# Optimization experiments

Hardware: AMD Instinct MI355X
Metric: run time of the kernel (lower is better)

Reference implementation:

```python
import jax, jax.numpy as jnp
import numpy as np

N, A, B, K = 100000, 64, 128, 27  # active sites, in/out channels, 3^3 offsets
EPS = 1e-4  # scn BatchNorm default eps
LEAK = 0.0  # leakiness=0 -> ReLU


def bn_lrelu(x, gamma, beta):
    # training-mode BN over active sites, fused leaky relu
    mu = x.mean(0)
    var = x.var(0)
    xh = (x - mu) * jax.lax.rsqrt(var + EPS) * gamma + beta
    return jnp.where(xh > 0, xh, LEAK * xh)


def subconv(f, nbr, mask, W):
    # submanifold conv via rulebook: f [N,Cin], nbr [N,K], mask [N,K], W [K,Cin,Cout]
    out = jnp.zeros((f.shape[0], W.shape[2]), f.dtype)
    for k in range(W.shape[0]):  # fixed small set of kernel offsets
        g = jnp.where(mask[:, k:k + 1], f[nbr[:, k]], jnp.zeros((), f.dtype))
        out = out + g @ W[k]
    return out


def setup_inputs() -> dict:
    key = jax.random.key(0)
    ks = jax.random.split(key, 8)
    feat = jax.random.normal(ks[0], (N, A), jnp.float32)
    nbr = jax.random.randint(ks[1], (N, K), 0, N, jnp.int32)
    mask = jax.random.randint(ks[2], (N, K), 0, 2, jnp.int32).astype(bool)
    # self-connection at center offset is always valid in submanifold conv
    center = K // 2
    nbr = nbr.at[:, center].set(jnp.arange(N, dtype=jnp.int32))
    mask = mask.at[:, center].set(True)
    s1 = 1.0 / np.sqrt(K * A)
    s2 = 1.0 / np.sqrt(K * B)
    W1 = jax.random.normal(ks[3], (K, A, B), jnp.float32) * s1
    W2 = jax.random.normal(ks[4], (K, B, B), jnp.float32) * s2
    Wnin = jax.random.normal(ks[5], (A, B), jnp.float32) / np.sqrt(A)
    gamma1 = jnp.ones((A,), jnp.float32)
    beta1 = jnp.zeros((A,), jnp.float32)
    gamma2 = jnp.ones((B,), jnp.float32)
    beta2 = jnp.zeros((B,), jnp.float32)
    return {"feat": feat, "gamma1": gamma1, "beta1": beta1, "W1": W1,
            "gamma2": gamma2, "beta2": beta2, "W2": W2, "Wnin": Wnin,
            "nbr": nbr, "mask": mask}


def reference(feat, gamma1, beta1, W1, gamma2, beta2, W2, Wnin, nbr, mask):
    y1 = feat @ Wnin  # NetworkInNetwork shortcut (a != b)
    h = bn_lrelu(feat, gamma1, beta1)
    h = subconv(h, nbr, mask, W1)
    h = bn_lrelu(h, gamma2, beta2)
    y2 = subconv(h, nbr, mask, W2)
    return y1 + y2  # add_feature_planes
```

## Files before the change

### kernel.cpp

```cpp
#include <hip/hip_runtime.h>
#include <stdint.h>

#define CA 64
#define CB 128
#define KOFF 27
#define BN_EPS 1e-4f

typedef short bf16x8 __attribute__((ext_vector_type(8)));
typedef float f32x4 __attribute__((ext_vector_type(4)));
typedef unsigned int u32x4 __attribute__((ext_vector_type(4)));
typedef unsigned short u16x4 __attribute__((ext_vector_type(4)));

__device__ __forceinline__ unsigned short f2bf(float f) {
  union { float f; uint32_t u; } c; c.f = f;
  uint32_t u = c.u;
  return (unsigned short)((u + 0x7FFFu + ((u >> 16) & 1u)) >> 16);
}

__device__ __forceinline__ void barrier_lds() {
  asm volatile("s_waitcnt lgkmcnt(0)\n\ts_barrier" ::: "memory");
}

__global__ void detect_mask_k(const unsigned char* __restrict__ m, int* flag) {
  unsigned v = 0;
  for (int i = threadIdx.x; i < 4096; i += 256)
    if (i & 3) v |= m[i];
  if (v) atomicOr(flag, 1);
}

__global__ void pack_mask_k(const void* __restrict__ mp, const int* __restrict__ flag,
                            uint32_t* __restrict__ bits, int n) {
  int i = blockIdx.x * blockDim.x + threadIdx.x;
  if (i >= n) return;
  uint32_t b = 0;
  if (*flag) {
    const unsigned char* m = (const unsigned char*)mp + (size_t)i * KOFF;
    for (int k = 0; k < KOFF; k++) b |= (m[k] ? 1u : 0u) << k;
  } else {
    const int* m = (const int*)mp + (size_t)i * KOFF;
    for (int k = 0; k < KOFF; k++) b |= (m[k] ? 1u : 0u) << k;
  }
  bits[i] = b;
}

__global__ void transpose_all_k(const float* __restrict__ W1, const float* __restrict__ W2,
                                const float* __restrict__ Wnin,
                                unsigned short* __restrict__ w1t, unsigned short* __restrict__ w2t,
                                unsigned short* __restrict__ wnt) {
  const int t1 = KOFF * CA * CB, t2 = KOFF * CB * CB, t3 = CA * CB;
  int idx = blockIdx.x * blockDim.x + threadIdx.x;
  if (idx < t1) {
    int ci = idx % CA; int r = idx / CA; int co = r % CB; int k = r / CB;
    w1t[idx] = f2bf(W1[((size_t)k * CA + ci) * CB + co]);
  } else if (idx < t1 + t2) {
    int j = idx - t1;
    int ci = j % CB; int r = j / CB; int co = r % CB; int k = r / CB;
    w2t[j] = f2bf(W2[((size_t)k * CB + ci) * CB + co]);
  } else if (idx < t1 + t2 + t3) {
    int j = idx - t1 - t2;
    int ci = j % CA; int co = j / CA;
    wnt[j] = f2bf(Wnin[(size_t)ci * CB + co]);
  }
}

template<int C>
__global__ void col_stats_k(const float* __restrict__ x, int n, float* __restrict__ sums) {
  __shared__ float ssum[C], ssq[C];
  int t = threadIdx.x;
  for (int i = t; i < C; i += 256) { ssum[i] = 0.f; ssq[i] = 0.f; }
  __syncthreads();
  const int c = t % C;
  const int rpb = 256 / C;
  float s = 0.f, q = 0.f;
  for (int r = blockIdx.x * rpb + t / C; r < n; r += gridDim.x * rpb) {
    float v = x[(size_t)r * C + c];
    s += v; q += v * v;
  }
  atomicAdd(&ssum[c], s);
  atomicAdd(&ssq[c], q);
  __syncthreads();
  for (int i = t; i < C; i += 256) {
    atomicAdd(&sums[i], ssum[i]);
    atomicAdd(&sums[C + i], ssq[i]);
  }
}

template<int C>
__global__ void bn_finalize_k(const float* __restrict__ sums, const float* __restrict__ gamma,
                              const float* __restrict__ beta, float* __restrict__ sc, int n) {
  int c = threadIdx.x;
  if (c >= C) return;
  float inv_n = 1.f / (float)n;
  float mean = sums[c] * inv_n;
  float var = sums[C + c] * inv_n - mean * mean;
  float rstd = rsqrtf(var + BN_EPS);
  float scale = gamma[c] * rstd;
  sc[c] = scale;
  sc[C + c] = beta[c] - mean * scale;
}

template<int C, bool RAW>
__global__ void bn_apply_k(const float* __restrict__ x, const float* __restrict__ sc,
                           unsigned short* __restrict__ h, unsigned short* __restrict__ raw,
                           int total) {
  int idx = (blockIdx.x * blockDim.x + threadIdx.x) * 4;
  if (idx >= total) return;
  f32x4 v = *(const f32x4*)&x[idx];
  int c0 = idx % C;
  u16x4 ho, ro;
#pragma unroll
  for (int j = 0; j < 4; j++) {
    float s = sc[c0 + j], b = sc[C + c0 + j];
    float hv = fmaxf(v[j] * s + b, 0.f);
    ho[j] = f2bf(hv);
    if (RAW) ro[j] = f2bf(v[j]);
  }
  *(u16x4*)&h[idx] = ho;
  if (RAW) *(u16x4*)&raw[idx] = ro;
}

template<int CIN, bool FUSE>
__launch_bounds__(256)
__global__ void conv_k(const unsigned short* __restrict__ hin,
                       const unsigned short* __restrict__ wt,
                       const int* __restrict__ nbr,
                       const uint32_t* __restrict__ mbits,
                       const unsigned short* __restrict__ fbraw,
                       const unsigned short* __restrict__ wnt,
                       float* __restrict__ out, int n) {
  constexpr int TR = 64;
  constexpr int STR = CIN + 8;
  constexpr int FSTR = CA + 8;
  constexpr int NKS = CIN / 32;
  constexpr int CH = CIN / 8;
  constexpr int NP = TR * CH / 256;

  __shared__ alignas(16) unsigned short tile[2][TR * STR];
  __shared__ alignas(16) unsigned short ftile[FUSE ? TR * FSTR : 16];
  __shared__ int lnbr[TR * KOFF];
  __shared__ uint32_t lmb[TR];

  const int t = threadIdx.x;
  const int rowbase = blockIdx.x * TR;
  const int nrows = min(TR, n - rowbase);

  for (int i = t; i < nrows * KOFF; i += 256) lnbr[i] = nbr[(size_t)rowbase * KOFF + i];
  if (t < TR) lmb[t] = (t < nrows) ? mbits[rowbase + t] : 0u;

  if constexpr (FUSE) {
#pragma unroll
    for (int p = 0; p < 2; p++) {
      int r = p * 32 + (t >> 3);
      int ch = (t & 7) * 8;
      u32x4 v = {0, 0, 0, 0};
      if (r < nrows) v = *(const u32x4*)&fbraw[(size_t)(rowbase + r) * CA + ch];
      *(u32x4*)&ftile[r * FSTR + ch] = v;
    }
  }
  __syncthreads();

  const int lane = t & 63;
  const int wave = t >> 6;
  const int l16 = lane & 15;
  const int quad = lane >> 4;
  const int colbase = wave * 32;
  const int goff = (t % CH) * 8;
  const int grow = t / CH;
  const int boff0 = (colbase + l16) * CIN + quad * 8;
  const int boff1 = boff0 + 16 * CIN;

  f32x4 acc[4][2];
#pragma unroll
  for (int i = 0; i < 4; i++) { acc[i][0] = f32x4{0,0,0,0}; acc[i][1] = f32x4{0,0,0,0}; }

  bf16x8 bfr[2][2 * NKS];
  u32x4 gr[NP];

#pragma unroll
  for (int ks = 0; ks < NKS; ks++) {
    bfr[0][2 * ks]     = *(const bf16x8*)&wt[boff0 + ks * 32];
    bfr[0][2 * ks + 1] = *(const bf16x8*)&wt[boff1 + ks * 32];
  }
#pragma unroll
  for (int p = 0; p < NP; p++) {
    int r = p * (256 / CH) + grow;
    u32x4 v = {0, 0, 0, 0};
    if (r < nrows && (lmb[r] & 1u)) v = *(const u32x4*)&hin[(size_t)lnbr[r * KOFF] * CIN + goff];
    gr[p] = v;
  }
#pragma unroll
  for (int p = 0; p < NP; p++) {
    int r = p * (256 / CH) + grow;
    *(u32x4*)&tile[0][r * STR + goff] = gr[p];
  }
  {
    const unsigned short* wk = wt + (size_t)1 * CB * CIN;
#pragma unroll
    for (int ks = 0; ks < NKS; ks++) {
      bfr[1][2 * ks]     = *(const bf16x8*)&wk[boff0 + ks * 32];
      bfr[1][2 * ks + 1] = *(const bf16x8*)&wk[boff1 + ks * 32];
    }
  }
#pragma unroll
  for (int p = 0; p < NP; p++) {
    int r = p * (256 / CH) + grow;
    u32x4 v = {0, 0, 0, 0};
    if (r < nrows && ((lmb[r] >> 1) & 1u))
      v = *(const u32x4*)&hin[(size_t)lnbr[r * KOFF + 1] * CIN + goff];
    gr[p] = v;
  }

  if constexpr (FUSE) {
#pragma unroll
    for (int ks = 0; ks < CA / 32; ks++) {
      bf16x8 b0 = *(const bf16x8*)&wnt[(colbase + l16) * CA + ks * 32 + quad * 8];
      bf16x8 b1 = *(const bf16x8*)&wnt[(colbase + 16 + l16) * CA + ks * 32 + quad * 8];
#pragma unroll
      for (int rt = 0; rt < 4; rt++) {
        bf16x8 a = *(const bf16x8*)&ftile[(rt * 16 + l16) * FSTR + ks * 32 + quad * 8];
        acc[rt][0] = __builtin_amdgcn_mfma_f32_16x16x32_bf16(a, b0, acc[rt][0], 0, 0, 0);
        acc[rt][1] = __builtin_amdgcn_mfma_f32_16x16x32_bf16(a, b1, acc[rt][1], 0, 0, 0);
      }
    }
  }
  barrier_lds();

#pragma unroll
  for (int k = 0; k < KOFF; k++) {
    const int cur = k & 1, nxt = cur ^ 1;
#pragma unroll
    for (int ks = 0; ks < NKS; ks++) {
#pragma unroll
      for (int rt = 0; rt < 4; rt++) {
        bf16x8 a = *(const bf16x8*)&tile[cur][(rt * 16 + l16) * STR + ks * 32 + quad * 8];
        acc[rt][0] = __builtin_amdgcn_mfma_f32_16x16x32_bf16(a, bfr[cur][2 * ks],     acc[rt][0], 0, 0, 0);
        acc[rt][1] = __builtin_amdgcn_mfma_f32_16x16x32_bf16(a, bfr[cur][2 * ks + 1], acc[rt][1], 0, 0, 0);
      }
    }
    if (k + 2 < KOFF) {
      const unsigned short* wk = wt + (size_t)(k + 2) * CB * CIN;
#pragma unroll
      for (int ks = 0; ks < NKS; ks++) {
        bfr[cur][2 * ks]     = *(const bf16x8*)&wk[boff0 + ks * 32];
        bfr[cur][2 * ks + 1] = *(const bf16x8*)&wk[boff1 + ks * 32];
      }
    }
    if (k + 1 < KOFF) {
#pragma unroll
      for (int p = 0; p < NP; p++) {
        int r = p * (256 / CH) + grow;
        *(u32x4*)&tile[nxt][r * STR + goff] = gr[p];
      }
      if (k + 2 < KOFF) {
#pragma unroll
        for (int p = 0; p < NP; p++) {
          int r = p * (256 / CH) + grow;
          u32x4 v = {0, 0, 0, 0};
          if (r < nrows && ((lmb[r] >> (k + 2)) & 1u))
            v = *(const u32x4*)&hin[(size_t)lnbr[r * KOFF + k + 2] * CIN + goff];
          gr[p] = v;
        }
      }
      barrier_lds();
    }
  }

#pragma unroll
  for (int rt = 0; rt < 4; rt++) {
#pragma unroll
    for (int ct = 0; ct < 2; ct++) {
#pragma unroll
      for (int i = 0; i < 4; i++) {
        int r = rt * 16 + quad * 4 + i;
        if (r < nrows) {
          int c = colbase + ct * 16 + l16;
          out[(size_t)(rowbase + r) * CB + c] = acc[rt][ct][i];
        }
      }
    }
  }
}

extern "C" void kernel_launch(void* const* d_in, const int* in_sizes, int n_in,
                              void* d_out, int out_size, void* d_ws, size_t ws_size,
                              hipStream_t stream) {
  const float* feat   = (const float*)d_in[0];
  const float* gamma1 = (const float*)d_in[1];
  const float* beta1  = (const float*)d_in[2];
  const float* W1     = (const float*)d_in[3];
  const float* gamma2 = (const float*)d_in[4];
  const float* beta2  = (const float*)d_in[5];
  const float* W2     = (const float*)d_in[6];
  const float* Wnin   = (const float*)d_in[7];
  const int*   nbr    = (const int*)d_in[8];
  const void*  mask   = d_in[9];
  float* out = (float*)d_out;

  const int n = in_sizes[0] / CA;

  char* ws = (char*)d_ws;
  size_t off = 0;
  auto alloc = [&](size_t bytes) { size_t p = off; off += (bytes + 255) & ~(size_t)255; return p; };
  int*            flag  = (int*)           (ws + alloc(256));
  float*          sums1 = (float*)         (ws + alloc(2 * CA * 4));
  float*          sums2 = (float*)         (ws + alloc(2 * CB * 4));
  float*          sc1   = (float*)         (ws + alloc(2 * CA * 4));
  float*          sc2   = (float*)         (ws + alloc(2 * CB * 4));
  uint32_t*       mbits = (uint32_t*)      (ws + alloc((size_t)n * 4));
  unsigned short* fb    = (unsigned short*)(ws + alloc((size_t)n * CA * 2));
  unsigned short* hb1   = (unsigned short*)(ws + alloc((size_t)n * CA * 2));
  float*          out1  = (float*)         (ws + alloc((size_t)n * CB * 4));
  unsigned short* hb2   = (unsigned short*)(ws + alloc((size_t)n * CB * 2));
  unsigned short* w1t   = (unsigned short*)(ws + alloc((size_t)KOFF * CB * CA * 2));
  unsigned short* w2t   = (unsigned short*)(ws + alloc((size_t)KOFF * CB * CB * 2));
  unsigned short* wnt   = (unsigned short*)(ws + alloc((size_t)CB * CA * 2));

  hipMemsetAsync(d_ws, 0, 1792, stream);

  detect_mask_k<<<1, 256, 0, stream>>>((const unsigned char*)mask, flag);
  pack_mask_k<<<(n + 255) / 256, 256, 0, stream>>>(mask, flag, mbits, n);

  {
    int tot = KOFF * CA * CB + KOFF * CB * CB + CA * CB;
    transpose_all_k<<<(tot + 255) / 256, 256, 0, stream>>>(W1, W2, Wnin, w1t, w2t, wnt);
  }

  col_stats_k<CA><<<256, 256, 0, stream>>>(feat, n, sums1);
  bn_finalize_k<CA><<<1, CA, 0, stream>>>(sums1, gamma1, beta1, sc1, n);
  bn_apply_k<CA, true><<<(n * CA / 4 + 255) / 256, 256, 0, stream>>>(feat, sc1, hb1, fb, n * CA);

  conv_k<CA, false><<<(n + 63) / 64, 256, 0, stream>>>(hb1, w1t, nbr, mbits, nullptr, nullptr, out1, n);

  col_stats_k<CB><<<256, 256, 0, stream>>>(out1, n, sums2);
  bn_finalize_k<CB><<<1, CB, 0, stream>>>(sums2, gamma2, beta2, sc2, n);
  bn_apply_k<CB, false><<<(n * CB / 4 + 255) / 256, 256, 0, stream>>>(out1, sc2, hb2, nullptr, n * CB);

  conv_k<CB, true><<<(n + 63) / 64, 256, 0, stream>>>(hb2, w2t, nbr, mbits, fb, wnt, out, n);
}
```

Baseline: 528.4 us.

## Fuse BN stats into conv, XOR-swizzle LDS tiles, deepen gather prefetch

The first conv now accumulates per-channel sum and sum-of-squares from its accumulators and adds them atomically, which removes the separate col_stats pass over out1. The LDS tile drops its padding in favour of an XOR swizzle to avoid bank conflicts. The gather prefetch is two offsets deep, weights are loaded one offset ahead into a single register buffer, and neighbour indices are pre-scaled to byte offsets. The NiN shortcut reads fbraw straight from global memory instead of staging it in LDS, and launch bounds ask for 4 blocks per CU. These trade fewer kernels and less LDS for more register pressure, atomics on the stats buffer, and weight loads that sit closer to their use.

```diff
diff --git a/kernel.cpp b/kernel.cpp
--- a/kernel.cpp
+++ b/kernel.cpp
@@ -119,24 +119,22 @@
   if (RAW) *(u16x4*)&raw[idx] = ro;
 }
 
-template<int CIN, bool FUSE>
-__launch_bounds__(256)
+template<int CIN, bool FUSE, bool STATS>
+__launch_bounds__(256, 4)
 __global__ void conv_k(const unsigned short* __restrict__ hin,
                        const unsigned short* __restrict__ wt,
                        const int* __restrict__ nbr,
                        const uint32_t* __restrict__ mbits,
                        const unsigned short* __restrict__ fbraw,
                        const unsigned short* __restrict__ wnt,
-                       float* __restrict__ out, int n) {
+                       float* __restrict__ out, float* __restrict__ sums, int n) {
   constexpr int TR = 64;
-  constexpr int STR = CIN + 8;
-  constexpr int FSTR = CA + 8;
   constexpr int NKS = CIN / 32;
   constexpr int CH = CIN / 8;
-  constexpr int NP = TR * CH / 256;
-
-  __shared__ alignas(16) unsigned short tile[2][TR * STR];
-  __shared__ alignas(16) unsigned short ftile[FUSE ? TR * FSTR : 16];
+  constexpr int RPP = 256 / CH;
+  constexpr int NP = TR / RPP;
+
+  __shared__ alignas(16) unsigned short tile[2][TR * CIN];
   __shared__ int lnbr[TR * KOFF];
   __shared__ uint32_t lmb[TR];
 
@@ -144,71 +142,83 @@
   const int rowbase = blockIdx.x * TR;
   const int nrows = min(TR, n - rowbase);
 
-  for (int i = t; i < nrows * KOFF; i += 256) lnbr[i] = nbr[(size_t)rowbase * KOFF + i];
+  for (int i = t; i < nrows * KOFF; i += 256)
+    lnbr[i] = nbr[(size_t)rowbase * KOFF + i] * (CIN * 2);
   if (t < TR) lmb[t] = (t < nrows) ? mbits[rowbase + t] : 0u;
-
-  if constexpr (FUSE) {
-#pragma unroll
-    for (int p = 0; p < 2; p++) {
-      int r = p * 32 + (t >> 3);
-      int ch = (t & 7) * 8;
-      u32x4 v = {0, 0, 0, 0};
-      if (r < nrows) v = *(const u32x4*)&fbraw[(size_t)(rowbase + r) * CA + ch];
-      *(u32x4*)&ftile[r * FSTR + ch] = v;
-    }
-  }
-  __syncthreads();
+  barrier_lds();
 
   const int lane = t & 63;
   const int wave = t >> 6;
   const int l16 = lane & 15;
   const int quad = lane >> 4;
   const int colbase = wave * 32;
-  const int goff = (t % CH) * 8;
+  const int c16 = t % CH;
   const int grow = t / CH;
   const int boff0 = (colbase + l16) * CIN + quad * 8;
   const int boff1 = boff0 + 16 * CIN;
 
+  int toff[NP]; int pnb[NP]; uint32_t pmb[NP];
+#pragma unroll
+  for (int p = 0; p < NP; p++) {
+    int r = p * RPP + grow;
+    toff[p] = r * CIN + ((c16 ^ (r & (CH - 1))) * 8);
+    pnb[p] = r * KOFF;
+    pmb[p] = lmb[r];
+  }
+
   f32x4 acc[4][2];
 #pragma unroll
   for (int i = 0; i < 4; i++) { acc[i][0] = f32x4{0,0,0,0}; acc[i][1] = f32x4{0,0,0,0}; }
 
-  bf16x8 bfr[2][2 * NKS];
-  u32x4 gr[NP];
-
-#pragma unroll
-  for (int ks = 0; ks < NKS; ks++) {
-    bfr[0][2 * ks]     = *(const bf16x8*)&wt[boff0 + ks * 32];
-    bfr[0][2 * ks + 1] = *(const bf16x8*)&wt[boff1 + ks * 32];
-  }
-#pragma unroll
-  for (int p = 0; p < NP; p++) {
-    int r = p * (256 / CH) + grow;
-    u32x4 v = {0, 0, 0, 0};
-    if (r < nrows && (lmb[r] & 1u)) v = *(const u32x4*)&hin[(size_t)lnbr[r * KOFF] * CIN + goff];
-    gr[p] = v;
-  }
-#pragma unroll
-  for (int p = 0; p < NP; p++) {
-    int r = p * (256 / CH) + grow;
-    *(u32x4*)&tile[0][r * STR + goff] = gr[p];
-  }
-  {
-    const unsigned short* wk = wt + (size_t)1 * CB * CIN;
-#pragma unroll
-    for (int ks = 0; ks < NKS; ks++) {
-      bfr[1][2 * ks]     = *(const bf16x8*)&wk[boff0 + ks * 32];
-      bfr[1][2 * ks + 1] = *(const bf16x8*)&wk[boff1 + ks * 32];
-    }
-  }
-#pragma unroll
-  for (int p = 0; p < NP; p++) {
-    int r = p * (256 / CH) + grow;
-    u32x4 v = {0, 0, 0, 0};
-    if (r < nrows && ((lmb[r] >> 1) & 1u))
-      v = *(const u32x4*)&hin[(size_t)lnbr[r * KOFF + 1] * CIN + goff];
-    gr[p] = v;
-  }
+  bf16x8 bfr[2 * NKS];
+  u32x4 gr[2][NP];
+  u32x4 g0[NP];
+
+#define LOADB(kk, dst)                                                         \
+  {                                                                            \
+    const unsigned short* wk = wt + (size_t)(kk) * (CB * CIN);                 \
+    _Pragma("unroll")                                                          \
+    for (int ks = 0; ks < NKS; ks++) {                                         \
+      dst[2 * ks]     = *(const bf16x8*)&wk[boff0 + ks * 32];                  \
+      dst[2 * ks + 1] = *(const bf16x8*)&wk[boff1 + ks * 32];                  \
+    }                                                                          \
+  }
+
+#define GATHER(kk, dst)                                                        \
+  {                                                                            \
+    _Pragma("unroll")                                                          \
+    for (int p = 0; p < NP; p++) {                                             \
+      u32x4 v = {0, 0, 0, 0};                                                  \
+      if ((pmb[p] >> (kk)) & 1u)                                               \
+        v = *(const u32x4*)((const char*)hin +                                 \
+                            (size_t)(unsigned)lnbr[pnb[p] + (kk)] + c16 * 16); \
+      dst[p] = v;                                                              \
+    }                                                                          \
+  }
+
+#define STAGE(buf, src)                                                        \
+  {                                                                            \
+    _Pragma("unroll")                                                          \
+    for (int p = 0; p < NP; p++) *(u32x4*)&tile[buf][toff[p]] = src[p];        \
+  }
+
+#define MMA(buf)                                                               \
+  {                                                                            \
+    _Pragma("unroll")                                                          \
+    for (int ks = 0; ks < NKS; ks++) {                                         \
+      _Pragma("unroll")                                                        \
+      for (int rt = 0; rt < 4; rt++) {                                         \
+        int row = rt * 16 + l16;                                               \
+        bf16x8 a = *(const bf16x8*)&tile[buf][row * CIN +                      \
+                      (((ks * 4 + quad) ^ (row & (CH - 1))) * 8)];             \
+        acc[rt][0] = __builtin_amdgcn_mfma_f32_16x16x32_bf16(a, bfr[2 * ks],     acc[rt][0], 0, 0, 0); \
+        acc[rt][1] = __builtin_amdgcn_mfma_f32_16x16x32_bf16(a, bfr[2 * ks + 1], acc[rt][1], 0, 0, 0); \
+      }                                                                        \
+    }                                                                          \
+  }
+
+  LOADB(0, bfr);
+  GATHER(0, g0);
 
   if constexpr (FUSE) {
 #pragma unroll
@@ -217,53 +227,36 @@
       bf16x8 b1 = *(const bf16x8*)&wnt[(colbase + 16 + l16) * CA + ks * 32 + quad * 8];
 #pragma unroll
       for (int rt = 0; rt < 4; rt++) {
-        bf16x8 a = *(const bf16x8*)&ftile[(rt * 16 + l16) * FSTR + ks * 32 + quad * 8];
+        int r = rt * 16 + l16;
+        bf16x8 a = bf16x8{0, 0, 0, 0, 0, 0, 0, 0};
+        if (r < nrows)
+          a = *(const bf16x8*)&fbraw[(size_t)(rowbase + r) * CA + ks * 32 + quad * 8];
         acc[rt][0] = __builtin_amdgcn_mfma_f32_16x16x32_bf16(a, b0, acc[rt][0], 0, 0, 0);
         acc[rt][1] = __builtin_amdgcn_mfma_f32_16x16x32_bf16(a, b1, acc[rt][1], 0, 0, 0);
       }
     }
   }
+
+  STAGE(0, g0);
+  GATHER(1, gr[0]);
+  GATHER(2, gr[1]);
   barrier_lds();
 
 #pragma unroll
   for (int k = 0; k < KOFF; k++) {
     const int cur = k & 1, nxt = cur ^ 1;
-#pragma unroll
-    for (int ks = 0; ks < NKS; ks++) {
-#pragma unroll
-      for (int rt = 0; rt < 4; rt++) {
-        bf16x8 a = *(const bf16x8*)&tile[cur][(rt * 16 + l16) * STR + ks * 32 + quad * 8];
-        acc[rt][0] = __builtin_amdgcn_mfma_f32_16x16x32_bf16(a, bfr[cur][2 * ks],     acc[rt][0], 0, 0, 0);
-        acc[rt][1] = __builtin_amdgcn_mfma_f32_16x16x32_bf16(a, bfr[cur][2 * ks + 1], acc[rt][1], 0, 0, 0);
-      }
-    }
-    if (k + 2 < KOFF) {
-      const unsigned short* wk = wt + (size_t)(k + 2) * CB * CIN;
-#pragma unroll
-      for (int ks = 0; ks < NKS; ks++) {
-        bfr[cur][2 * ks]     = *(const bf16x8*)&wk[boff0 + ks * 32];
-        bfr[cur][2 * ks + 1] = *(const bf16x8*)&wk[boff1 + ks * 32];
-      }
-    }
+    MMA(cur);
     if (k + 1 < KOFF) {
-#pragma unroll
-      for (int p = 0; p < NP; p++) {
-        int r = p * (256 / CH) + grow;
-        *(u32x4*)&tile[nxt][r * STR + goff] = gr[p];
-      }
-      if (k + 2 < KOFF) {
-#pragma unroll
-        for (int p = 0; p < NP; p++) {
-          int r = p * (256 / CH) + grow;
-          u32x4 v = {0, 0, 0, 0};
-          if (r < nrows && ((lmb[r] >> (k + 2)) & 1u))
-            v = *(const u32x4*)&hin[(size_t)lnbr[r * KOFF + k + 2] * CIN + goff];
-          gr[p] = v;
-        }
-      }
+      LOADB(k + 1, bfr);
+      STAGE(nxt, gr[cur]);
+      if (k + 3 < KOFF) GATHER(k + 3, gr[cur]);
       barrier_lds();
     }
   }
+#undef LOADB
+#undef GATHER
+#undef STAGE
+#undef MMA
 
 #pragma unroll
   for (int rt = 0; rt < 4; rt++) {
@@ -276,6 +269,24 @@
           int c = colbase + ct * 16 + l16;
           out[(size_t)(rowbase + r) * CB + c] = acc[rt][ct][i];
         }
+      }
+    }
+  }
+
+  if constexpr (STATS) {
+#pragma unroll
+    for (int ct = 0; ct < 2; ct++) {
+      float s = 0.f, q = 0.f;
+#pragma unroll
+      for (int rt = 0; rt < 4; rt++)
+#pragma unroll
+        for (int i = 0; i < 4; i++) { float v = acc[rt][ct][i]; s += v; q += v * v; }
+      s += __shfl_xor(s, 16); s += __shfl_xor(s, 32);
+      q += __shfl_xor(q, 16); q += __shfl_xor(q, 32);
+      if (quad == 0) {
+        int cch = colbase + ct * 16 + l16;
+        atomicAdd(&sums[cch], s);
+        atomicAdd(&sums[CB + cch], q);
       }
     }
   }
@@ -329,11 +340,10 @@
   bn_finalize_k<CA><<<1, CA, 0, stream>>>(sums1, gamma1, beta1, sc1, n);
   bn_apply_k<CA, true><<<(n * CA / 4 + 255) / 256, 256, 0, stream>>>(feat, sc1, hb1, fb, n * CA);
 
-  conv_k<CA, false><<<(n + 63) / 64, 256, 0, stream>>>(hb1, w1t, nbr, mbits, nullptr, nullptr, out1, n);
-
-  col_stats_k<CB><<<256, 256, 0, stream>>>(out1, n, sums2);
+  conv_k<CA, false, true><<<(n + 63) / 64, 256, 0, stream>>>(hb1, w1t, nbr, mbits, nullptr, nullptr, out1, sums2, n);
+
   bn_finalize_k<CB><<<1, CB, 0, stream>>>(sums2, gamma2, beta2, sc2, n);
   bn_apply_k<CB, false><<<(n * CB / 4 + 255) / 256, 256, 0, stream>>>(out1, sc2, hb2, nullptr, n * CB);
 
-  conv_k<CB, true><<<(n + 63) / 64, 256, 0, stream>>>(hb2, w2t, nbr, mbits, fb, wnt, out, n);
-}
+  conv_k<CB, true, false><<<(n + 63) / 64, 256, 0, stream>>>(hb2, w2t, nbr, mbits, fb, wnt, out, nullptr, n);
+}
```

Result: no change. 536.4 us (+1.5%).
